# Kernel tuning notes

Hardware: AMD Instinct MI355X
Metric: run time of the kernel (lower is better)

The kernel has to match this reference:

```python
import jax, jax.numpy as jnp
import numpy as np

N, C_IN, H, W = 48, 64, 128, 128


def _conv3x3(x, w, b):
    # NCHW conv, kernel 3, stride 1, pad 1 (SAME)
    y = jax.lax.conv_general_dilated(
        x, w, window_strides=(1, 1), padding=((1, 1), (1, 1)),
        dimension_numbers=("NCHW", "OIHW", "NCHW"))
    return y + b[None, :, None, None]


def setup_inputs() -> dict:
    key = jax.random.key(0)
    ks = jax.random.split(key, 4)
    s1 = 1.0 / np.sqrt(C_IN * 9)
    s2 = 1.0 / np.sqrt(128 * 9)
    s3 = 1.0 / np.sqrt(32 * 9)
    return {
        "x": jax.random.normal(ks[0], (N, C_IN, H, W), dtype=jnp.float32),
        "to_process": jnp.arange(N, dtype=jnp.int64) if jax.config.jax_enable_x64 else jnp.arange(N, dtype=jnp.int32),
        "batch_size": 8,
        "W1": jax.random.normal(ks[1], (128, C_IN, 3, 3), dtype=jnp.float32) * s1,
        "b1": jnp.zeros((128,), dtype=jnp.float32),
        "W2": jax.random.normal(ks[2], (32, 128, 3, 3), dtype=jnp.float32) * s2,
        "b2": jnp.zeros((32,), dtype=jnp.float32),
        "W3": jax.random.normal(ks[3], (1, 32, 3, 3), dtype=jnp.float32) * s3,
        "b3": jnp.zeros((1,), dtype=jnp.float32),
    }


def reference(x, to_process, batch_size, W1, b1, W2, b2, W3, b3):
    # x holds only the active sites listed in to_process; all ops are per-site.
    x = jax.nn.relu(_conv3x3(x, W1, b1))          # [N,128,H,W]
    x = jax.nn.relu(_conv3x3(x, W2, b2))          # [N,32,H,W]
    n, c, h, w = x.shape
    # SparseBilinearUpsample(2): half-pixel-center bilinear x2 (align_corners=False)
    x = jax.image.resize(x, (n, c, 2 * h, 2 * w), method="bilinear")
    x = _conv3x3(x, W3, b3)                        # [N,1,2H,2W]
    return x
```

## Files before the change

### kernel.cpp

```cpp
#include <hip/hip_runtime.h>


typedef _Float16 half_t;
typedef _Float16 half2_t __attribute__((ext_vector_type(2)));
typedef _Float16 half4_t __attribute__((ext_vector_type(4)));
typedef _Float16 half8   __attribute__((ext_vector_type(8)));
typedef float    floatx4  __attribute__((ext_vector_type(4)));
typedef float    floatx16 __attribute__((ext_vector_type(16)));

__global__ __launch_bounds__(256) void repack_w(
    const float* __restrict__ W1, const float* __restrict__ W2,
    const float* __restrict__ W3, half_t* __restrict__ wh1,
    half_t* __restrict__ wh2, half_t* __restrict__ wh3)
{
    int idx = blockIdx.x * 256 + threadIdx.x;
    if (idx < 73728) {
        int ci = idx & 63, co = (idx >> 6) & 127, tap = idx >> 13;
        wh1[idx] = (half_t)W1[(co * 64 + ci) * 9 + tap];
    } else if (idx < 110592) {
        int j = idx - 73728;
        int ci = j & 127, co = (j >> 7) & 31, tap = j >> 12;
        wh2[j] = (half_t)W2[(co * 128 + ci) * 9 + tap];
    } else if (idx < 110880) {
        int j = idx - 110592;
        int ci = j & 31, tap = j >> 5;
        wh3[j] = (half_t)W3[ci * 9 + tap];
    }
}

__global__ __launch_bounds__(256) void repack_x(
    const float* __restrict__ x, half_t* __restrict__ xh)
{
    const int tid = threadIdx.x;
    const int px = tid & 127, rr = tid >> 7;
    const int y = blockIdx.x * 2 + rr;
    const int n = blockIdx.y;
    const float* xn = x + (size_t)n * 64 * 16384 + (size_t)y * 128 + px;
    half2_t hb[32];
#pragma unroll
    for (int c2 = 0; c2 < 32; ++c2) {
        float f0 = xn[(size_t)(2 * c2) * 16384];
        float f1 = xn[(size_t)(2 * c2 + 1) * 16384];
        half2_t h; h.x = (half_t)f0; h.y = (half_t)f1;
        hb[c2] = h;
    }
    half_t* op = xh + (((size_t)n * 128 + y) * 128 + px) * 64;
#pragma unroll
    for (int k = 0; k < 8; ++k)
        *(half8*)(op + k * 8) = *(half8*)(&hb[k * 4]);
}

__global__ __launch_bounds__(256, 2) void conv1_mfma(
    const half_t* __restrict__ xh,
    const half_t* __restrict__ wh,
    const float*  __restrict__ bias,
    half_t* __restrict__ y1h)
{
    __shared__ half_t lx[10 * 34 * 72];
    const int tid  = threadIdx.x;
    const int lane = tid & 63;
    const int wave = tid >> 6;
    const int l31 = lane & 31, lq = lane >> 5;
    const int wco = wave >> 1, wpx = wave & 1;
    const int x0 = blockIdx.x * 32, y0 = blockIdx.y * 8;
    const int n = blockIdx.z;
    const half_t* xn = xh + (size_t)n * (128 * 128 * 64);

    for (int idx = tid; idx < 10 * 34 * 8; idx += 256) {
        int ch = idx & 7;
        int col = (idx >> 3) % 34;
        int row = (idx >> 3) / 34;
        int gx = x0 - 1 + col, gy = y0 - 1 + row;
        half8 v = {};
        if ((unsigned)gx < 128u && (unsigned)gy < 128u)
            v = *(const half8*)(xn + ((size_t)gy * 128 + gx) * 64 + ch * 8);
        *(half8*)(&lx[(row * 34 + col) * 72 + ch * 8]) = v;
    }

    const half_t* wbase = wh + (wco * 64 + l31) * 64 + lq * 8;

    half8 w[2][8];
#pragma unroll
    for (int k = 0; k < 4; ++k) {
        w[0][2 * k]     = *(const half8*)(wbase + k * 16);
        w[0][2 * k + 1] = *(const half8*)(wbase + 32 * 64 + k * 16);
    }

    __syncthreads();

    floatx16 acc[2][4] = {};

#pragma unroll
    for (int tap = 0; tap < 9; ++tap) {
        const int dy = tap / 3, dx = tap % 3;
        const int cur = tap & 1, nxt = cur ^ 1;
        if (tap < 8) {
            const half_t* wn = wbase + (tap + 1) * (128 * 64);
#pragma unroll
            for (int k = 0; k < 4; ++k) {
                w[nxt][2 * k]     = *(const half8*)(wn + k * 16);
                w[nxt][2 * k + 1] = *(const half8*)(wn + 32 * 64 + k * 16);
            }
        }
        const half_t* bp = &lx[((wpx * 4 + dy) * 34 + l31 + dx) * 72 + lq * 8];
#pragma unroll
        for (int kc = 0; kc < 4; ++kc) {
            half8 b[4];
#pragma unroll
            for (int nf = 0; nf < 4; ++nf)
                b[nf] = *(const half8*)(bp + nf * (34 * 72) + kc * 16);
#pragma unroll
            for (int nf = 0; nf < 4; ++nf) {
                acc[0][nf] = __builtin_amdgcn_mfma_f32_32x32x16_f16(w[cur][2 * kc],     b[nf], acc[0][nf], 0, 0, 0);
                acc[1][nf] = __builtin_amdgcn_mfma_f32_32x32x16_f16(w[cur][2 * kc + 1], b[nf], acc[1][nf], 0, 0, 0);
            }
        }
    }

#pragma unroll
    for (int mf = 0; mf < 2; ++mf) {
        int co0 = wco * 64 + mf * 32 + lq * 4;
#pragma unroll
        for (int nf = 0; nf < 4; ++nf) {
            floatx16 A = acc[mf][nf];
            int oy = y0 + wpx * 4 + nf, ox = x0 + l31;
            half_t* op = y1h + (((size_t)n * 128 + oy) * 128 + ox) * 128 + co0;
#pragma unroll
            for (int g = 0; g < 4; ++g) {
                floatx4 bv = *(const floatx4*)(bias + co0 + 8 * g);
                half4_t o;
                o.x = (half_t)fmaxf(A[4 * g + 0] + bv.x, 0.f);
                o.y = (half_t)fmaxf(A[4 * g + 1] + bv.y, 0.f);
                o.z = (half_t)fmaxf(A[4 * g + 2] + bv.z, 0.f);
                o.w = (half_t)fmaxf(A[4 * g + 3] + bv.w, 0.f);
                *(half4_t*)(op + 8 * g) = o;
            }
        }
    }
}

__global__ __launch_bounds__(256, 3) void conv2_mfma(
    const half_t* __restrict__ y1h,
    const half_t* __restrict__ wh,
    const float*  __restrict__ bias,
    half_t* __restrict__ y2h)
{
    __shared__ half_t lx[18 * 34 * 40];
    const int tid  = threadIdx.x;
    const int lane = tid & 63;
    const int w    = tid >> 6;
    const int l15 = lane & 15, quad = lane >> 4;
    const int x0 = blockIdx.x * 32, y0 = blockIdx.y * 16;
    const int n = blockIdx.z;
    const half_t* yn = y1h + (size_t)n * (128 * 128 * 128);

    floatx4 acc[2][8] = {};

    for (int h = 0; h < 4; ++h) {
        for (int idx = tid; idx < 18 * 34 * 4; idx += 256) {
            int ch = idx & 3;
            int col = (idx >> 2) % 34;
            int row = (idx >> 2) / 34;
            int gx = x0 - 1 + col, gy = y0 - 1 + row;
            half8 v = {};
            if ((unsigned)gx < 128u && (unsigned)gy < 128u)
                v = *(const half8*)(yn + ((size_t)gy * 128 + gx) * 128 + h * 32 + ch * 8);
            *(half8*)(&lx[(row * 34 + col) * 40 + ch * 8]) = v;
        }
        __syncthreads();
#pragma unroll
        for (int tap = 0; tap < 9; ++tap) {
            const int dy = tap / 3, dx = tap % 3;
            const half_t* wt = wh + tap * (32 * 128) + l15 * 128 + h * 32 + quad * 8;
            half8 a0 = *(const half8*)(wt);
            half8 a1 = *(const half8*)(wt + 16 * 128);
#pragma unroll
            for (int nf = 0; nf < 8; ++nf) {
                int rr = w * 4 + (nf >> 1) + dy;
                int cc = (nf & 1) * 16 + l15 + dx;
                half8 b = *(const half8*)(&lx[(rr * 34 + cc) * 40 + quad * 8]);
                acc[0][nf] = __builtin_amdgcn_mfma_f32_16x16x32_f16(a0, b, acc[0][nf], 0, 0, 0);
                acc[1][nf] = __builtin_amdgcn_mfma_f32_16x16x32_f16(a1, b, acc[1][nf], 0, 0, 0);
            }
        }
        __syncthreads();
    }

#pragma unroll
    for (int mf = 0; mf < 2; ++mf) {
        int co0 = mf * 16 + quad * 4;
        floatx4 bv = *(const floatx4*)(bias + co0);
#pragma unroll
        for (int nf = 0; nf < 8; ++nf) {
            int oy = y0 + w * 4 + (nf >> 1), ox = x0 + (nf & 1) * 16 + l15;
            floatx4 A = acc[mf][nf];
            half4_t o;
            o.x = (half_t)fmaxf(A.x + bv.x, 0.f);
            o.y = (half_t)fmaxf(A.y + bv.y, 0.f);
            o.z = (half_t)fmaxf(A.z + bv.z, 0.f);
            o.w = (half_t)fmaxf(A.w + bv.w, 0.f);
            *(half4_t*)(y2h + (((size_t)n * 128 + oy) * 128 + ox) * 32 + co0) = o;
        }
    }
}

__global__ __launch_bounds__(256) void conv3_fused(
    const half_t* __restrict__ y2h,
    const half_t* __restrict__ wh3,
    const float*  __restrict__ bias,
    float* __restrict__ out)
{
    __shared__ half_t lu[10 * 34 * 40];
    const int tid = threadIdx.x;
    const int c = tid & 31, r = tid >> 5;
    const int x0 = blockIdx.x * 32, y0 = blockIdx.y * 8;
    const int n = blockIdx.z;
    const half_t* base = y2h + (size_t)n * (128 * 128 * 32);

    for (int idx = tid; idx < 10 * 34 * 4; idx += 256) {
        int cc = idx & 3;
        int p  = idx >> 2;
        int col = p % 34, row = p / 34;
        int X = x0 - 1 + col, Y = y0 - 1 + row;
        half8 o = {};
        if ((unsigned)X < 256u && (unsigned)Y < 256u) {
            int jx = X >> 1, jy = Y >> 1;
            int jxo = (X & 1) ? (jx < 127 ? jx + 1 : 127) : (jx > 0 ? jx - 1 : 0);
            int jyo = (Y & 1) ? (jy < 127 ? jy + 1 : 127) : (jy > 0 ? jy - 1 : 0);
            const half_t* p00 = base + ((size_t)jy  * 128 + jx ) * 32 + cc * 8;
            const half_t* p01 = base + ((size_t)jy  * 128 + jxo) * 32 + cc * 8;
            const half_t* p10 = base + ((size_t)jyo * 128 + jx ) * 32 + cc * 8;
            const half_t* p11 = base + ((size_t)jyo * 128 + jxo) * 32 + cc * 8;
            half8 v00 = *(const half8*)p00;
            half8 v01 = *(const half8*)p01;
            half8 v10 = *(const half8*)p10;
            half8 v11 = *(const half8*)p11;
            o = v00 * (half_t)0.5625f + (v01 + v10) * (half_t)0.1875f
              + v11 * (half_t)0.0625f;
        }
        *(half8*)(&lu[(row * 34 + col) * 40 + cc * 8]) = o;
    }
    __syncthreads();

    float acc = 0.f;
#pragma unroll
    for (int tap = 0; tap < 9; ++tap) {
        const int dy = tap / 3, dx = tap % 3;
        const half_t* lp = &lu[((r + dy) * 34 + c + dx) * 40];
        const half_t* wp = wh3 + tap * 32;
#pragma unroll
        for (int cc = 0; cc < 4; ++cc) {
            half8 v = *(const half8*)(lp + cc * 8);
            half8 w = *(const half8*)(wp + cc * 8);
            acc = __builtin_amdgcn_fdot2(__builtin_shufflevector(v, v, 0, 1),
                                         __builtin_shufflevector(w, w, 0, 1), acc, false);
            acc = __builtin_amdgcn_fdot2(__builtin_shufflevector(v, v, 2, 3),
                                         __builtin_shufflevector(w, w, 2, 3), acc, false);
            acc = __builtin_amdgcn_fdot2(__builtin_shufflevector(v, v, 4, 5),
                                         __builtin_shufflevector(w, w, 4, 5), acc, false);
            acc = __builtin_amdgcn_fdot2(__builtin_shufflevector(v, v, 6, 7),
                                         __builtin_shufflevector(w, w, 6, 7), acc, false);
        }
    }
    out[((size_t)n * 256 + (y0 + r)) * 256 + x0 + c] = acc + bias[0];
}

extern "C" void kernel_launch(void* const* d_in, const int* in_sizes, int n_in,
                              void* d_out, int out_size, void* d_ws, size_t ws_size,
                              hipStream_t stream) {
    const float* x  = (const float*)d_in[0];
    const float* W1 = (const float*)d_in[3];
    const float* b1 = (const float*)d_in[4];
    const float* W2 = (const float*)d_in[5];
    const float* b2 = (const float*)d_in[6];
    const float* W3 = (const float*)d_in[7];
    const float* b3 = (const float*)d_in[8];
    float* out = (float*)d_out;

    char* ws = (char*)d_ws;
    half_t* xh  = (half_t*)ws;
    half_t* y1h = (half_t*)(ws + 201326592ull);
    half_t* y2h = (half_t*)(ws + 402653184ull);
    half_t* wh1 = (half_t*)(ws + 452984832ull);
    half_t* wh2 = wh1 + 73728;
    half_t* wh3 = wh2 + 36864;

    repack_w<<<434, 256, 0, stream>>>(W1, W2, W3, wh1, wh2, wh3);
    repack_x<<<dim3(64, 48), 256, 0, stream>>>(x, xh);
    conv1_mfma<<<dim3(4, 16, 48), 256, 0, stream>>>(xh, wh1, b1, y1h);
    conv2_mfma<<<dim3(4, 8, 48), 256, 0, stream>>>(y1h, wh2, b2, y2h);
    conv3_fused<<<dim3(8, 32, 48), 256, 0, stream>>>(y2h, wh3, b3, out);
}
```

Baseline: 746.1 us.

## Shrink conv1 tile to 4 rows and drop weight register double-buffering

Halves the conv1 block tile from 8 output rows to 4, which cuts the LDS halo buffer, raises the occupancy hint from 2 to 3 blocks, and doubles the grid. The register double-buffered weight prefetch is removed, and weights are now loaded directly from global memory inside the kc loop. The aim is lower register and LDS pressure so more waves can hide latency. In exchange, each weight load now feeds half as many MFMAs, the halo overhead per output row grows, and weight load latency is no longer overlapped explicitly.

```diff
diff --git a/kernel.cpp b/kernel.cpp
--- a/kernel.cpp
+++ b/kernel.cpp
@@ -50,23 +50,23 @@
         *(half8*)(op + k * 8) = *(half8*)(&hb[k * 4]);
 }
 
-__global__ __launch_bounds__(256, 2) void conv1_mfma(
+__global__ __launch_bounds__(256, 3) void conv1_mfma(
     const half_t* __restrict__ xh,
     const half_t* __restrict__ wh,
     const float*  __restrict__ bias,
     half_t* __restrict__ y1h)
 {
-    __shared__ half_t lx[10 * 34 * 72];
+    __shared__ half_t lx[6 * 34 * 72];
     const int tid  = threadIdx.x;
     const int lane = tid & 63;
     const int wave = tid >> 6;
     const int l31 = lane & 31, lq = lane >> 5;
     const int wco = wave >> 1, wpx = wave & 1;
-    const int x0 = blockIdx.x * 32, y0 = blockIdx.y * 8;
+    const int x0 = blockIdx.x * 32, y0 = blockIdx.y * 4;
     const int n = blockIdx.z;
     const half_t* xn = xh + (size_t)n * (128 * 128 * 64);
 
-    for (int idx = tid; idx < 10 * 34 * 8; idx += 256) {
+    for (int idx = tid; idx < 6 * 34 * 8; idx += 256) {
         int ch = idx & 7;
         int col = (idx >> 3) % 34;
         int row = (idx >> 3) / 34;
@@ -76,44 +76,25 @@
             v = *(const half8*)(xn + ((size_t)gy * 128 + gx) * 64 + ch * 8);
         *(half8*)(&lx[(row * 34 + col) * 72 + ch * 8]) = v;
     }
-
-    const half_t* wbase = wh + (wco * 64 + l31) * 64 + lq * 8;
-
-    half8 w[2][8];
-#pragma unroll
-    for (int k = 0; k < 4; ++k) {
-        w[0][2 * k]     = *(const half8*)(wbase + k * 16);
-        w[0][2 * k + 1] = *(const half8*)(wbase + 32 * 64 + k * 16);
-    }
-
     __syncthreads();
 
-    floatx16 acc[2][4] = {};
+    floatx16 acc[2][2] = {};
 
 #pragma unroll
     for (int tap = 0; tap < 9; ++tap) {
         const int dy = tap / 3, dx = tap % 3;
-        const int cur = tap & 1, nxt = cur ^ 1;
-        if (tap < 8) {
-            const half_t* wn = wbase + (tap + 1) * (128 * 64);
-#pragma unroll
-            for (int k = 0; k < 4; ++k) {
-                w[nxt][2 * k]     = *(const half8*)(wn + k * 16);
-                w[nxt][2 * k + 1] = *(const half8*)(wn + 32 * 64 + k * 16);
-            }
-        }
-        const half_t* bp = &lx[((wpx * 4 + dy) * 34 + l31 + dx) * 72 + lq * 8];
+        const half_t* wt = wh + tap * (128 * 64) + (wco * 64 + l31) * 64 + lq * 8;
+        const half_t* bp = &lx[((wpx * 2 + dy) * 34 + l31 + dx) * 72 + lq * 8];
 #pragma unroll
         for (int kc = 0; kc < 4; ++kc) {
-            half8 b[4];
-#pragma unroll
-            for (int nf = 0; nf < 4; ++nf)
-                b[nf] = *(const half8*)(bp + nf * (34 * 72) + kc * 16);
-#pragma unroll
-            for (int nf = 0; nf < 4; ++nf) {
-                acc[0][nf] = __builtin_amdgcn_mfma_f32_32x32x16_f16(w[cur][2 * kc],     b[nf], acc[0][nf], 0, 0, 0);
-                acc[1][nf] = __builtin_amdgcn_mfma_f32_32x32x16_f16(w[cur][2 * kc + 1], b[nf], acc[1][nf], 0, 0, 0);
-            }
+            half8 a0 = *(const half8*)(wt + kc * 16);
+            half8 a1 = *(const half8*)(wt + 32 * 64 + kc * 16);
+            half8 b0 = *(const half8*)(bp + kc * 16);
+            half8 b1 = *(const half8*)(bp + 34 * 72 + kc * 16);
+            acc[0][0] = __builtin_amdgcn_mfma_f32_32x32x16_f16(a0, b0, acc[0][0], 0, 0, 0);
+            acc[1][0] = __builtin_amdgcn_mfma_f32_32x32x16_f16(a1, b0, acc[1][0], 0, 0, 0);
+            acc[0][1] = __builtin_amdgcn_mfma_f32_32x32x16_f16(a0, b1, acc[0][1], 0, 0, 0);
+            acc[1][1] = __builtin_amdgcn_mfma_f32_32x32x16_f16(a1, b1, acc[1][1], 0, 0, 0);
         }
     }
 
@@ -121,9 +102,9 @@
     for (int mf = 0; mf < 2; ++mf) {
         int co0 = wco * 64 + mf * 32 + lq * 4;
 #pragma unroll
-        for (int nf = 0; nf < 4; ++nf) {
+        for (int nf = 0; nf < 2; ++nf) {
             floatx16 A = acc[mf][nf];
-            int oy = y0 + wpx * 4 + nf, ox = x0 + l31;
+            int oy = y0 + wpx * 2 + nf, ox = x0 + l31;
             half_t* op = y1h + (((size_t)n * 128 + oy) * 128 + ox) * 128 + co0;
 #pragma unroll
             for (int g = 0; g < 4; ++g) {
@@ -287,7 +268,7 @@
 
     repack_w<<<434, 256, 0, stream>>>(W1, W2, W3, wh1, wh2, wh3);
     repack_x<<<dim3(64, 48), 256, 0, stream>>>(x, xh);
-    conv1_mfma<<<dim3(4, 16, 48), 256, 0, stream>>>(xh, wh1, b1, y1h);
+    conv1_mfma<<<dim3(4, 32, 48), 256, 0, stream>>>(xh, wh1, b1, y1h);
     conv2_mfma<<<dim3(4, 8, 48), 256, 0, stream>>>(y1h, wh2, b2, y2h);
     conv3_fused<<<dim3(8, 32, 48), 256, 0, stream>>>(y2h, wh3, b3, out);
 }
```

Measured after the change: 833.7 us. 11.7% more time.
